# Optimization experiments

Hardware: AMD Instinct MI355X
Metric: run time of the kernel (lower is better)

Reference implementation:

```python
import jax, jax.numpy as jnp
import numpy as np

GROUP_SIZE = 32

def setup_inputs() -> dict:
    key = jax.random.key(0)
    k_x, k_w, k_b, k_se, k_zp = jax.random.split(key, 5)
    B, S, IN_CH, OUT_CH = 4, 2048, 4096, 4096
    n_groups = IN_CH // GROUP_SIZE
    x = jax.random.normal(k_x, (B, S, IN_CH), dtype=jnp.float32)
    weight = jax.random.normal(k_w, (OUT_CH, IN_CH), dtype=jnp.float32) * 0.02
    bias = jax.random.normal(k_b, (OUT_CH,), dtype=jnp.float32)
    # po2 scale: 2**e with int8 exponent; pick exponents so scale ~ weight magnitude / 15
    exp = jax.random.randint(k_se, (OUT_CH, n_groups, 1), -10, -6).astype(jnp.float32)
    weight_scale = jnp.exp2(exp)  # float32
    weight_zp = jax.random.randint(k_zp, (OUT_CH, n_groups, 1), 0, 16).astype(jnp.float32)
    return {"x": x, "weight": weight, "bias": bias,
            "weight_scale": weight_scale, "weight_zp": weight_zp}

def reference(x, weight, bias, weight_scale, weight_zp):
    out_ch, in_ch = weight.shape
    # [O, n_groups, group_size]
    w_g = weight.reshape(out_ch, in_ch // GROUP_SIZE, GROUP_SIZE)
    # asym uint4 quantize: clamp(round(w/scale + zp), 0, 15)
    q = jnp.clip(jnp.round(w_g / weight_scale + weight_zp), 0.0, 15.0)
    # dequantize: (q - zp) * scale, flatten groups back to [O, I]
    dq = ((q - weight_zp) * weight_scale).reshape(out_ch, in_ch)
    # F.linear: x @ dq.T + bias
    return jnp.einsum('bsi,oi->bso', x, dq) + bias
```

## Files before the change

### kernel.cpp

```cpp
#include <hip/hip_runtime.h>
#include <hip/hip_bf16.h>
#include <stdint.h>

typedef unsigned short ushort_t;
typedef __bf16 bf16x8 __attribute__((ext_vector_type(8)));
typedef float f32x4 __attribute__((ext_vector_type(4)));
typedef ushort_t ushort8v __attribute__((ext_vector_type(8)));


__device__ __forceinline__ ushort_t f2bf(float f) {
  unsigned int u = __float_as_uint(f);
  u += 0x7FFFu + ((u >> 16) & 1u);
  return (ushort_t)(u >> 16);
}

typedef __attribute__((address_space(1))) void gvoid_t;
typedef __attribute__((address_space(3))) void lvoid_t;

__device__ __forceinline__ void async_cp16(const ushort_t* g, ushort_t* l) {
  __builtin_amdgcn_global_load_lds((gvoid_t*)g, (lvoid_t*)l, 16, 0, 0);
}


__global__ __launch_bounds__(256) void cvt_x_kernel(const float4* __restrict__ x,
                                                    ushort8v* __restrict__ xb, int n8) {
  int i = blockIdx.x * 256 + threadIdx.x;
  if (i >= n8) return;
  float4 a = x[2 * i], b = x[2 * i + 1];
  ushort8v o;
  o[0] = f2bf(a.x); o[1] = f2bf(a.y); o[2] = f2bf(a.z); o[3] = f2bf(a.w);
  o[4] = f2bf(b.x); o[5] = f2bf(b.y); o[6] = f2bf(b.z); o[7] = f2bf(b.w);
  xb[i] = o;
}


__device__ __forceinline__ float dq1(float w, float rs, float s, float z) {
  float q = rintf(w * rs + z);
  q = fminf(fmaxf(q, 0.0f), 15.0f);
  return (q - z) * s;
}

__global__ __launch_bounds__(256) void dequant_w_kernel(const float* __restrict__ w,
                                                        const float* __restrict__ sc,
                                                        const float* __restrict__ zp,
                                                        ushort8v* __restrict__ wq, int n8) {
  int i = blockIdx.x * 256 + threadIdx.x;
  if (i >= n8) return;
  int base = i * 8;
  int gi = base >> 5;
  float s = sc[gi], z = zp[gi];
  float rs = 1.0f / s;
  const float4* w4 = (const float4*)(w + base);
  float4 a = w4[0], b = w4[1];
  ushort8v o;
  o[0] = f2bf(dq1(a.x, rs, s, z)); o[1] = f2bf(dq1(a.y, rs, s, z));
  o[2] = f2bf(dq1(a.z, rs, s, z)); o[3] = f2bf(dq1(a.w, rs, s, z));
  o[4] = f2bf(dq1(b.x, rs, s, z)); o[5] = f2bf(dq1(b.y, rs, s, z));
  o[6] = f2bf(dq1(b.z, rs, s, z)); o[7] = f2bf(dq1(b.w, rs, s, z));
  wq[i] = o;
}


#define BM 256
#define BN 256
#define BK 64

__device__ __forceinline__ f32x4 mfma16(bf16x8 a, bf16x8 b, f32x4 c) {
  return __builtin_amdgcn_mfma_f32_16x16x32_bf16(a, b, c, 0, 0, 0);
}

template <int MH, int NHB>
__device__ __forceinline__ void mfma_quad(f32x4 acc[2][4][4], const bf16x8 Afr[4][2],
                                          const bf16x8 Bfr[4][2]) {
#pragma unroll
  for (int k = 0; k < 2; ++k)
#pragma unroll
    for (int mt = 0; mt < 4; ++mt)
#pragma unroll
      for (int nt = 0; nt < 2; ++nt)
        acc[MH][mt][NHB * 2 + nt] =
            mfma16(Afr[mt][k], Bfr[NHB * 2 + nt][k], acc[MH][mt][NHB * 2 + nt]);
}

__global__ __launch_bounds__(512, 2) void gemm_bt_bias_kernel(
    const ushort_t* __restrict__ A,
    const ushort_t* __restrict__ B,
    const float* __restrict__ bias,
    float* __restrict__ C,
    int M, int N, int K) {
  __shared__ ushort_t sA[2][BM * BK];
  __shared__ ushort_t sB[2][BN * BK];

  const int tid  = threadIdx.x;
  const int wave = tid >> 6;
  const int lane = tid & 63;
  const int l15 = lane & 15, l4 = lane >> 4;

  int wg = blockIdx.x;
  const int nwg = gridDim.x;
  if ((nwg & 7) == 0) wg = (wg & 7) * (nwg >> 3) + (wg >> 3);
  const int nbn = N / BN;
  const int m0 = (wg / nbn) * BM, n0 = (wg % nbn) * BN;
  const int wm = (wave >> 2) * 128, wn = (wave & 3) * 64;

  const int srow = tid >> 3;
  const int scol = ((tid & 7) ^ (srow & 7)) * 8;
  const int ldst = wave * 64 * 8;

  const int xa  = l15 & 7;
  const int pc0 = (l4 ^ xa) << 3;
  const int pc1 = ((4 + l4) ^ xa) << 3;
  const int aoff = (wm + l15) * BK;
  const int boff = (wn + l15) * BK;

  f32x4 acc[2][4][4] = {};
  bf16x8 Afr[4][2], Bfr[4][2];

#define STAGE_A(sb, s, kn) \
  async_cp16(A + (size_t)(m0 + (s) * 64 + srow) * K + (kn) + scol, &sA[sb][(s) * 4096 + ldst])
#define STAGE_B(sb, s, kn) \
  async_cp16(B + (size_t)(n0 + (s) * 64 + srow) * K + (kn) + scol, &sB[sb][(s) * 4096 + ldst])
#define LDA(rb, mh, mt, k) \
  (*(const bf16x8*)&sA[rb][aoff + ((mh) * 64 + (mt) * 16) * BK + ((k) ? pc1 : pc0)])
#define LDB(rb, nt, k) \
  (*(const bf16x8*)&sB[rb][boff + (nt) * 16 * BK + ((k) ? pc1 : pc0)])
#define BAR()   __builtin_amdgcn_s_barrier()
#define LGKM0() asm volatile("s_waitcnt lgkmcnt(0)" ::: "memory")
#define VM(n)   asm volatile("s_waitcnt vmcnt(" #n ")" ::: "memory")
#define PRIO(p) __builtin_amdgcn_s_setprio(p)

  STAGE_B(0, 0, 0); STAGE_B(0, 1, 0); STAGE_A(0, 0, 0);
  STAGE_B(0, 2, 0); STAGE_B(0, 3, 0); STAGE_A(0, 2, 0);
  STAGE_A(0, 1, 0); STAGE_A(0, 3, 0);
  VM(2);
  BAR();

  const int nK = K / BK;
#pragma unroll 2
  for (int t = 0; t < nK - 1; ++t) {
    const int rb = t & 1, sb = rb ^ 1;
    const int kn = (t + 1) * BK;
#pragma unroll
    for (int mt = 0; mt < 4; ++mt) { Afr[mt][0] = LDA(rb, 0, mt, 0); Afr[mt][1] = LDA(rb, 0, mt, 1); }
#pragma unroll
    for (int nt = 0; nt < 2; ++nt) { Bfr[nt][0] = LDB(rb, nt, 0); Bfr[nt][1] = LDB(rb, nt, 1); }
    STAGE_B(sb, 0, kn); STAGE_B(sb, 1, kn); STAGE_A(sb, 0, kn);
    BAR(); LGKM0();
    PRIO(1); mfma_quad<0, 0>(acc, Afr, Bfr); PRIO(0);
    BAR();
#pragma unroll
    for (int nt = 2; nt < 4; ++nt) { Bfr[nt][0] = LDB(rb, nt, 0); Bfr[nt][1] = LDB(rb, nt, 1); }
    STAGE_B(sb, 2, kn); STAGE_B(sb, 3, kn); STAGE_A(sb, 2, kn);
    BAR(); LGKM0();
    PRIO(1); mfma_quad<0, 1>(acc, Afr, Bfr); PRIO(0);
    VM(6);
    BAR();
#pragma unroll
    for (int mt = 0; mt < 4; ++mt) { Afr[mt][0] = LDA(rb, 1, mt, 0); Afr[mt][1] = LDA(rb, 1, mt, 1); }
    STAGE_A(sb, 1, kn); STAGE_A(sb, 3, kn);
    BAR(); LGKM0();
    PRIO(1); mfma_quad<1, 0>(acc, Afr, Bfr); PRIO(0);
    BAR();
    PRIO(1); mfma_quad<1, 1>(acc, Afr, Bfr); PRIO(0);
    VM(2);
    BAR();
  }

  {
    const int rb = (nK - 1) & 1;
#pragma unroll
    for (int mt = 0; mt < 4; ++mt) { Afr[mt][0] = LDA(rb, 0, mt, 0); Afr[mt][1] = LDA(rb, 0, mt, 1); }
#pragma unroll
    for (int nt = 0; nt < 2; ++nt) { Bfr[nt][0] = LDB(rb, nt, 0); Bfr[nt][1] = LDB(rb, nt, 1); }
    BAR(); LGKM0();
    PRIO(1); mfma_quad<0, 0>(acc, Afr, Bfr); PRIO(0);
    BAR();
#pragma unroll
    for (int nt = 2; nt < 4; ++nt) { Bfr[nt][0] = LDB(rb, nt, 0); Bfr[nt][1] = LDB(rb, nt, 1); }
    BAR(); LGKM0();
    PRIO(1); mfma_quad<0, 1>(acc, Afr, Bfr); PRIO(0);
    VM(0);
    BAR();
#pragma unroll
    for (int mt = 0; mt < 4; ++mt) { Afr[mt][0] = LDA(rb, 1, mt, 0); Afr[mt][1] = LDA(rb, 1, mt, 1); }
    BAR(); LGKM0();
    PRIO(1); mfma_quad<1, 0>(acc, Afr, Bfr); PRIO(0);
    BAR();
    PRIO(1); mfma_quad<1, 1>(acc, Afr, Bfr); PRIO(0);
  }

  const int ccol = n0 + wn + l15;
  const int crow = m0 + wm + l4 * 4;
#pragma unroll
  for (int nt = 0; nt < 4; ++nt) {
    const float bv = bias[ccol + nt * 16];
#pragma unroll
    for (int mh = 0; mh < 2; ++mh)
#pragma unroll
      for (int mt = 0; mt < 4; ++mt)
#pragma unroll
        for (int r = 0; r < 4; ++r)
          C[(size_t)(crow + mh * 64 + mt * 16 + r) * N + ccol + nt * 16] =
              acc[mh][mt][nt][r] + bv;
  }
}


extern "C" void kernel_launch(void* const* d_in, const int* in_sizes, int n_in,
                              void* d_out, int out_size, void* d_ws, size_t ws_size,
                              hipStream_t stream) {
  const float* x    = (const float*)d_in[0];
  const float* w    = (const float*)d_in[1];
  const float* bias = (const float*)d_in[2];
  const float* sc   = (const float*)d_in[3];
  const float* zp   = (const float*)d_in[4];
  float* out = (float*)d_out;

  const int N = in_sizes[2];
  const int K = in_sizes[1] / N;
  const int M = in_sizes[0] / K;

  ushort_t* xb = (ushort_t*)d_ws;
  ushort_t* wq = xb + (size_t)M * K;

  int xn8 = (M * K) / 8;
  cvt_x_kernel<<<(xn8 + 255) / 256, 256, 0, stream>>>((const float4*)x, (ushort8v*)xb, xn8);

  int wn8 = (N * K) / 8;
  dequant_w_kernel<<<(wn8 + 255) / 256, 256, 0, stream>>>(w, sc, zp, (ushort8v*)wq, wn8);

  dim3 grid((M / BM) * (N / BN));
  gemm_bt_bias_kernel<<<grid, 512, 0, stream>>>(xb, wq, bias, out, M, N, K);
}
```

Baseline: 539.4 us.

## Prefetch two K-tiles ahead in GEMM and merge prep kernels into one

The GEMM main loop now issues global-to-LDS loads for tile t+2 into the buffer just consumed, instead of loading tile t+1 into the other buffer. This gives memory requests more time to land and reorders the vmcnt waits to match. The two preprocessing kernels are also merged into one grid-stride kernel with a fixed 2048-block grid, which removes a launch. A risk is that writing into the buffer currently being read depends on barrier placement; if that ordering is wrong it can race.

```diff
diff --git a/kernel.cpp b/kernel.cpp
--- a/kernel.cpp
+++ b/kernel.cpp
@@ -21,43 +21,42 @@
   __builtin_amdgcn_global_load_lds((gvoid_t*)g, (lvoid_t*)l, 16, 0, 0);
 }
 
-
-__global__ __launch_bounds__(256) void cvt_x_kernel(const float4* __restrict__ x,
-                                                    ushort8v* __restrict__ xb, int n8) {
-  int i = blockIdx.x * 256 + threadIdx.x;
-  if (i >= n8) return;
-  float4 a = x[2 * i], b = x[2 * i + 1];
-  ushort8v o;
-  o[0] = f2bf(a.x); o[1] = f2bf(a.y); o[2] = f2bf(a.z); o[3] = f2bf(a.w);
-  o[4] = f2bf(b.x); o[5] = f2bf(b.y); o[6] = f2bf(b.z); o[7] = f2bf(b.w);
-  xb[i] = o;
-}
-
-
 __device__ __forceinline__ float dq1(float w, float rs, float s, float z) {
   float q = rintf(w * rs + z);
   q = fminf(fmaxf(q, 0.0f), 15.0f);
   return (q - z) * s;
 }
 
-__global__ __launch_bounds__(256) void dequant_w_kernel(const float* __restrict__ w,
-                                                        const float* __restrict__ sc,
-                                                        const float* __restrict__ zp,
-                                                        ushort8v* __restrict__ wq, int n8) {
-  int i = blockIdx.x * 256 + threadIdx.x;
-  if (i >= n8) return;
-  int base = i * 8;
-  int gi = base >> 5;
-  float s = sc[gi], z = zp[gi];
-  float rs = 1.0f / s;
-  const float4* w4 = (const float4*)(w + base);
-  float4 a = w4[0], b = w4[1];
-  ushort8v o;
-  o[0] = f2bf(dq1(a.x, rs, s, z)); o[1] = f2bf(dq1(a.y, rs, s, z));
-  o[2] = f2bf(dq1(a.z, rs, s, z)); o[3] = f2bf(dq1(a.w, rs, s, z));
-  o[4] = f2bf(dq1(b.x, rs, s, z)); o[5] = f2bf(dq1(b.y, rs, s, z));
-  o[6] = f2bf(dq1(b.z, rs, s, z)); o[7] = f2bf(dq1(b.w, rs, s, z));
-  wq[i] = o;
+
+__global__ __launch_bounds__(256) void prep_kernel(
+    const float4* __restrict__ x, ushort8v* __restrict__ xb, int xn8,
+    const float* __restrict__ w, const float* __restrict__ sc,
+    const float* __restrict__ zp, ushort8v* __restrict__ wq, int wn8) {
+  const int total = xn8 + wn8;
+  const int stride = gridDim.x * 256;
+  for (int i = blockIdx.x * 256 + threadIdx.x; i < total; i += stride) {
+    if (i < xn8) {
+      float4 a = x[2 * i], b = x[2 * i + 1];
+      ushort8v o;
+      o[0] = f2bf(a.x); o[1] = f2bf(a.y); o[2] = f2bf(a.z); o[3] = f2bf(a.w);
+      o[4] = f2bf(b.x); o[5] = f2bf(b.y); o[6] = f2bf(b.z); o[7] = f2bf(b.w);
+      xb[i] = o;
+    } else {
+      int j = i - xn8;
+      int base = j * 8;
+      int gi = base >> 5;
+      float s = sc[gi], z = zp[gi];
+      float rs = 1.0f / s;
+      const float4* w4 = (const float4*)(w + base);
+      float4 a = w4[0], b = w4[1];
+      ushort8v o;
+      o[0] = f2bf(dq1(a.x, rs, s, z)); o[1] = f2bf(dq1(a.y, rs, s, z));
+      o[2] = f2bf(dq1(a.z, rs, s, z)); o[3] = f2bf(dq1(a.w, rs, s, z));
+      o[4] = f2bf(dq1(b.x, rs, s, z)); o[5] = f2bf(dq1(b.y, rs, s, z));
+      o[6] = f2bf(dq1(b.z, rs, s, z)); o[7] = f2bf(dq1(b.w, rs, s, z));
+      wq[j] = o;
+    }
+  }
 }
 
 
@@ -129,35 +128,64 @@
 #define VM(n)   asm volatile("s_waitcnt vmcnt(" #n ")" ::: "memory")
 #define PRIO(p) __builtin_amdgcn_s_setprio(p)
 
-  STAGE_B(0, 0, 0); STAGE_B(0, 1, 0); STAGE_A(0, 0, 0);
-  STAGE_B(0, 2, 0); STAGE_B(0, 3, 0); STAGE_A(0, 2, 0);
-  STAGE_A(0, 1, 0); STAGE_A(0, 3, 0);
-  VM(2);
+#define LOAD_A_MH0(rb) \
+  _Pragma("unroll") for (int mt = 0; mt < 4; ++mt) { Afr[mt][0] = LDA(rb, 0, mt, 0); Afr[mt][1] = LDA(rb, 0, mt, 1); }
+#define LOAD_A_MH1(rb) \
+  _Pragma("unroll") for (int mt = 0; mt < 4; ++mt) { Afr[mt][0] = LDA(rb, 1, mt, 0); Afr[mt][1] = LDA(rb, 1, mt, 1); }
+#define LOAD_B_LO(rb) \
+  _Pragma("unroll") for (int nt = 0; nt < 2; ++nt) { Bfr[nt][0] = LDB(rb, nt, 0); Bfr[nt][1] = LDB(rb, nt, 1); }
+#define LOAD_B_HI(rb) \
+  _Pragma("unroll") for (int nt = 2; nt < 4; ++nt) { Bfr[nt][0] = LDB(rb, nt, 0); Bfr[nt][1] = LDB(rb, nt, 1); }
+
+  STAGE_A(0, 0, 0);  STAGE_A(0, 2, 0);
+  STAGE_B(0, 0, 0);  STAGE_B(0, 1, 0);  STAGE_B(0, 2, 0);  STAGE_B(0, 3, 0);
+  STAGE_A(0, 1, 0);  STAGE_A(0, 3, 0);
+  STAGE_A(1, 0, BK); STAGE_A(1, 2, BK);
+  STAGE_B(1, 0, BK); STAGE_B(1, 1, BK); STAGE_B(1, 2, BK); STAGE_B(1, 3, BK);
+  STAGE_A(1, 1, BK); STAGE_A(1, 3, BK);
+  VM(10);
   BAR();
 
   const int nK = K / BK;
 #pragma unroll 2
-  for (int t = 0; t < nK - 1; ++t) {
-    const int rb = t & 1, sb = rb ^ 1;
-    const int kn = (t + 1) * BK;
-#pragma unroll
-    for (int mt = 0; mt < 4; ++mt) { Afr[mt][0] = LDA(rb, 0, mt, 0); Afr[mt][1] = LDA(rb, 0, mt, 1); }
-#pragma unroll
-    for (int nt = 0; nt < 2; ++nt) { Bfr[nt][0] = LDB(rb, nt, 0); Bfr[nt][1] = LDB(rb, nt, 1); }
-    STAGE_B(sb, 0, kn); STAGE_B(sb, 1, kn); STAGE_A(sb, 0, kn);
+  for (int t = 0; t < nK - 2; ++t) {
+    const int rb = t & 1;
+    const int kn2 = (t + 2) * BK;
+    LOAD_A_MH0(rb);
+    LOAD_B_LO(rb);
     BAR(); LGKM0();
     PRIO(1); mfma_quad<0, 0>(acc, Afr, Bfr); PRIO(0);
     BAR();
-#pragma unroll
-    for (int nt = 2; nt < 4; ++nt) { Bfr[nt][0] = LDB(rb, nt, 0); Bfr[nt][1] = LDB(rb, nt, 1); }
-    STAGE_B(sb, 2, kn); STAGE_B(sb, 3, kn); STAGE_A(sb, 2, kn);
+    LOAD_B_HI(rb);
+    STAGE_A(rb, 0, kn2); STAGE_A(rb, 2, kn2);
     BAR(); LGKM0();
     PRIO(1); mfma_quad<0, 1>(acc, Afr, Bfr); PRIO(0);
-    VM(6);
-    BAR();
-#pragma unroll
-    for (int mt = 0; mt < 4; ++mt) { Afr[mt][0] = LDA(rb, 1, mt, 0); Afr[mt][1] = LDA(rb, 1, mt, 1); }
-    STAGE_A(sb, 1, kn); STAGE_A(sb, 3, kn);
+    VM(10);
+    BAR();
+    LOAD_A_MH1(rb);
+    STAGE_B(rb, 0, kn2); STAGE_B(rb, 1, kn2); STAGE_B(rb, 2, kn2); STAGE_B(rb, 3, kn2);
+    BAR(); LGKM0();
+    PRIO(1); mfma_quad<1, 0>(acc, Afr, Bfr); PRIO(0);
+    BAR();
+    STAGE_A(rb, 1, kn2); STAGE_A(rb, 3, kn2);
+    PRIO(1); mfma_quad<1, 1>(acc, Afr, Bfr); PRIO(0);
+    VM(10);
+    BAR();
+  }
+
+  {
+    const int rb = (nK - 2) & 1;
+    LOAD_A_MH0(rb);
+    LOAD_B_LO(rb);
+    BAR(); LGKM0();
+    PRIO(1); mfma_quad<0, 0>(acc, Afr, Bfr); PRIO(0);
+    BAR();
+    LOAD_B_HI(rb);
+    BAR(); LGKM0();
+    PRIO(1); mfma_quad<0, 1>(acc, Afr, Bfr); PRIO(0);
+    VM(8);
+    BAR();
+    LOAD_A_MH1(rb);
     BAR(); LGKM0();
     PRIO(1); mfma_quad<1, 0>(acc, Afr, Bfr); PRIO(0);
     BAR();
@@ -165,24 +193,19 @@
     VM(2);
     BAR();
   }
-
   {
     const int rb = (nK - 1) & 1;
-#pragma unroll
-    for (int mt = 0; mt < 4; ++mt) { Afr[mt][0] = LDA(rb, 0, mt, 0); Afr[mt][1] = LDA(rb, 0, mt, 1); }
-#pragma unroll
-    for (int nt = 0; nt < 2; ++nt) { Bfr[nt][0] = LDB(rb, nt, 0); Bfr[nt][1] = LDB(rb, nt, 1); }
+    LOAD_A_MH0(rb);
+    LOAD_B_LO(rb);
     BAR(); LGKM0();
     PRIO(1); mfma_quad<0, 0>(acc, Afr, Bfr); PRIO(0);
     BAR();
-#pragma unroll
-    for (int nt = 2; nt < 4; ++nt) { Bfr[nt][0] = LDB(rb, nt, 0); Bfr[nt][1] = LDB(rb, nt, 1); }
+    LOAD_B_HI(rb);
     BAR(); LGKM0();
     PRIO(1); mfma_quad<0, 1>(acc, Afr, Bfr); PRIO(0);
     VM(0);
     BAR();
-#pragma unroll
-    for (int mt = 0; mt < 4; ++mt) { Afr[mt][0] = LDA(rb, 1, mt, 0); Afr[mt][1] = LDA(rb, 1, mt, 1); }
+    LOAD_A_MH1(rb);
     BAR(); LGKM0();
     PRIO(1); mfma_quad<1, 0>(acc, Afr, Bfr); PRIO(0);
     BAR();
@@ -224,10 +247,9 @@
   ushort_t* wq = xb + (size_t)M * K;
 
   int xn8 = (M * K) / 8;
-  cvt_x_kernel<<<(xn8 + 255) / 256, 256, 0, stream>>>((const float4*)x, (ushort8v*)xb, xn8);
-
   int wn8 = (N * K) / 8;
-  dequant_w_kernel<<<(wn8 + 255) / 256, 256, 0, stream>>>(w, sc, zp, (ushort8v*)wq, wn8);
+  prep_kernel<<<2048, 256, 0, stream>>>((const float4*)x, (ushort8v*)xb, xn8,
+                                        w, sc, zp, (ushort8v*)wq, wn8);
 
   dim3 grid((M / BM) * (N / BN));
   gemm_bt_bias_kernel<<<grid, 512, 0, stream>>>(xb, wq, bias, out, M, N, K);
```

Result: slower. 600.0 us (+11.2%).

## Simplify GEMM main loop to one barrier per K-step and widen conversion kernels

Applied to the files above, without the earlier changes.

The GEMM inner loop drops the fine-grained interleaving of partial async stages and multiple barriers per K tile. It now waits for all prior copies, does one barrier, issues the full next-tile prefetch, then loads fragments and runs all MFMA quads back to back. The x-convert and weight-dequant kernels each handle 16 elements per thread instead of 8, which halves the thread count. The simpler schedule removes barrier overhead but may expose global-load latency, since it waits on vmcnt(0) every iteration and no longer staggers LDS reads around the MFMAs.

```diff
diff --git a/kernel.cpp b/kernel.cpp
--- a/kernel.cpp
+++ b/kernel.cpp
@@ -23,14 +23,16 @@
 
 
 __global__ __launch_bounds__(256) void cvt_x_kernel(const float4* __restrict__ x,
-                                                    ushort8v* __restrict__ xb, int n8) {
+                                                    ushort8v* __restrict__ xb, int n16) {
   int i = blockIdx.x * 256 + threadIdx.x;
-  if (i >= n8) return;
-  float4 a = x[2 * i], b = x[2 * i + 1];
-  ushort8v o;
-  o[0] = f2bf(a.x); o[1] = f2bf(a.y); o[2] = f2bf(a.z); o[3] = f2bf(a.w);
-  o[4] = f2bf(b.x); o[5] = f2bf(b.y); o[6] = f2bf(b.z); o[7] = f2bf(b.w);
-  xb[i] = o;
+  if (i >= n16) return;
+  float4 a = x[4 * i], b = x[4 * i + 1], c = x[4 * i + 2], d = x[4 * i + 3];
+  ushort8v o0, o1;
+  o0[0] = f2bf(a.x); o0[1] = f2bf(a.y); o0[2] = f2bf(a.z); o0[3] = f2bf(a.w);
+  o0[4] = f2bf(b.x); o0[5] = f2bf(b.y); o0[6] = f2bf(b.z); o0[7] = f2bf(b.w);
+  o1[0] = f2bf(c.x); o1[1] = f2bf(c.y); o1[2] = f2bf(c.z); o1[3] = f2bf(c.w);
+  o1[4] = f2bf(d.x); o1[5] = f2bf(d.y); o1[6] = f2bf(d.z); o1[7] = f2bf(d.w);
+  xb[2 * i] = o0; xb[2 * i + 1] = o1;
 }
 
 
@@ -43,21 +45,26 @@
 __global__ __launch_bounds__(256) void dequant_w_kernel(const float* __restrict__ w,
                                                         const float* __restrict__ sc,
                                                         const float* __restrict__ zp,
-                                                        ushort8v* __restrict__ wq, int n8) {
+                                                        ushort8v* __restrict__ wq, int n16) {
   int i = blockIdx.x * 256 + threadIdx.x;
-  if (i >= n8) return;
-  int base = i * 8;
+  if (i >= n16) return;
+  int base = i * 16;
   int gi = base >> 5;
   float s = sc[gi], z = zp[gi];
   float rs = 1.0f / s;
   const float4* w4 = (const float4*)(w + base);
-  float4 a = w4[0], b = w4[1];
-  ushort8v o;
-  o[0] = f2bf(dq1(a.x, rs, s, z)); o[1] = f2bf(dq1(a.y, rs, s, z));
-  o[2] = f2bf(dq1(a.z, rs, s, z)); o[3] = f2bf(dq1(a.w, rs, s, z));
-  o[4] = f2bf(dq1(b.x, rs, s, z)); o[5] = f2bf(dq1(b.y, rs, s, z));
-  o[6] = f2bf(dq1(b.z, rs, s, z)); o[7] = f2bf(dq1(b.w, rs, s, z));
-  wq[i] = o;
+  float4 a = w4[0], b = w4[1], c = w4[2], d = w4[3];
+  ushort8v o0, o1;
+  o0[0] = f2bf(dq1(a.x, rs, s, z)); o0[1] = f2bf(dq1(a.y, rs, s, z));
+  o0[2] = f2bf(dq1(a.z, rs, s, z)); o0[3] = f2bf(dq1(a.w, rs, s, z));
+  o0[4] = f2bf(dq1(b.x, rs, s, z)); o0[5] = f2bf(dq1(b.y, rs, s, z));
+  o0[6] = f2bf(dq1(b.z, rs, s, z)); o0[7] = f2bf(dq1(b.w, rs, s, z));
+  o1[0] = f2bf(dq1(c.x, rs, s, z)); o1[1] = f2bf(dq1(c.y, rs, s, z));
+  o1[2] = f2bf(dq1(c.z, rs, s, z)); o1[3] = f2bf(dq1(c.w, rs, s, z));
+  o1[4] = f2bf(dq1(d.x, rs, s, z)); o1[5] = f2bf(dq1(d.y, rs, s, z));
+  o1[6] = f2bf(dq1(d.z, rs, s, z)); o1[7] = f2bf(dq1(d.w, rs, s, z));
+  ushort8v* out8 = (ushort8v*)wq + 2 * i;
+  out8[0] = o0; out8[1] = o1;
 }
 
 
@@ -120,72 +127,52 @@
   async_cp16(A + (size_t)(m0 + (s) * 64 + srow) * K + (kn) + scol, &sA[sb][(s) * 4096 + ldst])
 #define STAGE_B(sb, s, kn) \
   async_cp16(B + (size_t)(n0 + (s) * 64 + srow) * K + (kn) + scol, &sB[sb][(s) * 4096 + ldst])
+#define STAGE_ALL(sb, kn) do { \
+  STAGE_A(sb, 0, kn); STAGE_A(sb, 1, kn); STAGE_A(sb, 2, kn); STAGE_A(sb, 3, kn); \
+  STAGE_B(sb, 0, kn); STAGE_B(sb, 1, kn); STAGE_B(sb, 2, kn); STAGE_B(sb, 3, kn); \
+} while (0)
 #define LDA(rb, mh, mt, k) \
   (*(const bf16x8*)&sA[rb][aoff + ((mh) * 64 + (mt) * 16) * BK + ((k) ? pc1 : pc0)])
 #define LDB(rb, nt, k) \
   (*(const bf16x8*)&sB[rb][boff + (nt) * 16 * BK + ((k) ? pc1 : pc0)])
 #define BAR()   __builtin_amdgcn_s_barrier()
-#define LGKM0() asm volatile("s_waitcnt lgkmcnt(0)" ::: "memory")
-#define VM(n)   asm volatile("s_waitcnt vmcnt(" #n ")" ::: "memory")
+#define VM0()   asm volatile("s_waitcnt vmcnt(0)" ::: "memory")
 #define PRIO(p) __builtin_amdgcn_s_setprio(p)
 
-  STAGE_B(0, 0, 0); STAGE_B(0, 1, 0); STAGE_A(0, 0, 0);
-  STAGE_B(0, 2, 0); STAGE_B(0, 3, 0); STAGE_A(0, 2, 0);
-  STAGE_A(0, 1, 0); STAGE_A(0, 3, 0);
-  VM(2);
-  BAR();
+#define LOAD_A_MH0(rb) \
+  _Pragma("unroll") for (int mt = 0; mt < 4; ++mt) { Afr[mt][0] = LDA(rb, 0, mt, 0); Afr[mt][1] = LDA(rb, 0, mt, 1); }
+#define LOAD_A_MH1(rb) \
+  _Pragma("unroll") for (int mt = 0; mt < 4; ++mt) { Afr[mt][0] = LDA(rb, 1, mt, 0); Afr[mt][1] = LDA(rb, 1, mt, 1); }
+#define LOAD_B_ALL(rb) \
+  _Pragma("unroll") for (int nt = 0; nt < 4; ++nt) { Bfr[nt][0] = LDB(rb, nt, 0); Bfr[nt][1] = LDB(rb, nt, 1); }
+
+  STAGE_ALL(0, 0);
 
   const int nK = K / BK;
 #pragma unroll 2
   for (int t = 0; t < nK - 1; ++t) {
-    const int rb = t & 1, sb = rb ^ 1;
-    const int kn = (t + 1) * BK;
-#pragma unroll
-    for (int mt = 0; mt < 4; ++mt) { Afr[mt][0] = LDA(rb, 0, mt, 0); Afr[mt][1] = LDA(rb, 0, mt, 1); }
-#pragma unroll
-    for (int nt = 0; nt < 2; ++nt) { Bfr[nt][0] = LDB(rb, nt, 0); Bfr[nt][1] = LDB(rb, nt, 1); }
-    STAGE_B(sb, 0, kn); STAGE_B(sb, 1, kn); STAGE_A(sb, 0, kn);
-    BAR(); LGKM0();
+    const int rb = t & 1;
+    VM0();
+    BAR();
+    STAGE_ALL(rb ^ 1, (t + 1) * BK);
+    LOAD_A_MH0(rb);
+    LOAD_B_ALL(rb);
     PRIO(1); mfma_quad<0, 0>(acc, Afr, Bfr); PRIO(0);
-    BAR();
-#pragma unroll
-    for (int nt = 2; nt < 4; ++nt) { Bfr[nt][0] = LDB(rb, nt, 0); Bfr[nt][1] = LDB(rb, nt, 1); }
-    STAGE_B(sb, 2, kn); STAGE_B(sb, 3, kn); STAGE_A(sb, 2, kn);
-    BAR(); LGKM0();
     PRIO(1); mfma_quad<0, 1>(acc, Afr, Bfr); PRIO(0);
-    VM(6);
-    BAR();
-#pragma unroll
-    for (int mt = 0; mt < 4; ++mt) { Afr[mt][0] = LDA(rb, 1, mt, 0); Afr[mt][1] = LDA(rb, 1, mt, 1); }
-    STAGE_A(sb, 1, kn); STAGE_A(sb, 3, kn);
-    BAR(); LGKM0();
+    LOAD_A_MH1(rb);
     PRIO(1); mfma_quad<1, 0>(acc, Afr, Bfr); PRIO(0);
-    BAR();
     PRIO(1); mfma_quad<1, 1>(acc, Afr, Bfr); PRIO(0);
-    VM(2);
-    BAR();
   }
-
   {
     const int rb = (nK - 1) & 1;
-#pragma unroll
-    for (int mt = 0; mt < 4; ++mt) { Afr[mt][0] = LDA(rb, 0, mt, 0); Afr[mt][1] = LDA(rb, 0, mt, 1); }
-#pragma unroll
-    for (int nt = 0; nt < 2; ++nt) { Bfr[nt][0] = LDB(rb, nt, 0); Bfr[nt][1] = LDB(rb, nt, 1); }
-    BAR(); LGKM0();
+    VM0();
+    BAR();
+    LOAD_A_MH0(rb);
+    LOAD_B_ALL(rb);
     PRIO(1); mfma_quad<0, 0>(acc, Afr, Bfr); PRIO(0);
-    BAR();
-#pragma unroll
-    for (int nt = 2; nt < 4; ++nt) { Bfr[nt][0] = LDB(rb, nt, 0); Bfr[nt][1] = LDB(rb, nt, 1); }
-    BAR(); LGKM0();
     PRIO(1); mfma_quad<0, 1>(acc, Afr, Bfr); PRIO(0);
-    VM(0);
-    BAR();
-#pragma unroll
-    for (int mt = 0; mt < 4; ++mt) { Afr[mt][0] = LDA(rb, 1, mt, 0); Afr[mt][1] = LDA(rb, 1, mt, 1); }
-    BAR(); LGKM0();
+    LOAD_A_MH1(rb);
     PRIO(1); mfma_quad<1, 0>(acc, Afr, Bfr); PRIO(0);
-    BAR();
     PRIO(1); mfma_quad<1, 1>(acc, Afr, Bfr); PRIO(0);
   }
 
@@ -223,11 +210,11 @@
   ushort_t* xb = (ushort_t*)d_ws;
   ushort_t* wq = xb + (size_t)M * K;
 
-  int xn8 = (M * K) / 8;
-  cvt_x_kernel<<<(xn8 + 255) / 256, 256, 0, stream>>>((const float4*)x, (ushort8v*)xb, xn8);
-
-  int wn8 = (N * K) / 8;
-  dequant_w_kernel<<<(wn8 + 255) / 256, 256, 0, stream>>>(w, sc, zp, (ushort8v*)wq, wn8);
+  int xn16 = (M * K) / 16;
+  cvt_x_kernel<<<(xn16 + 255) / 256, 256, 0, stream>>>((const float4*)x, (ushort8v*)xb, xn16);
+
+  int wn16 = (N * K) / 16;
+  dequant_w_kernel<<<(wn16 + 255) / 256, 256, 0, stream>>>(w, sc, zp, (ushort8v*)wq, wn16);
 
   dim3 grid((M / BM) * (N / BN));
   gemm_bt_bias_kernel<<<grid, 512, 0, stream>>>(xb, wq, bias, out, M, N, K);
```

Result: slower. 568.6 us (+5.4%).

## Switch GEMM to 32x32x16 MFMA with 4 waves and 128x128 warp tiles

Applied to the files above, without the earlier changes.

Rewrites the bf16 GEMM main loop to use 32x32x16 MFMA instructions, with 256 threads per block and each wave owning a 128x128 output tile instead of 8 waves of 128x64. The K loop becomes a simpler double-buffered schedule: wait for all loads, barrier, issue the next tile's async copies, then interleave LDS fragment reads with MFMA groups using lgkmcnt waits and sched barriers. The aim is higher MFMA throughput per LDS byte read and fewer barriers per iteration. In exchange it needs many more accumulator registers (256 floats per lane) and runs only one block of 4 waves per CU, and the full vmcnt(0) wait at the top of each iteration reduces how much the global loads overlap with compute.

```diff
diff --git a/kernel.cpp b/kernel.cpp
--- a/kernel.cpp
+++ b/kernel.cpp
@@ -4,7 +4,7 @@
 
 typedef unsigned short ushort_t;
 typedef __bf16 bf16x8 __attribute__((ext_vector_type(8)));
-typedef float f32x4 __attribute__((ext_vector_type(4)));
+typedef float f32x16 __attribute__((ext_vector_type(16)));
 typedef ushort_t ushort8v __attribute__((ext_vector_type(8)));
 
 
@@ -65,24 +65,7 @@
 #define BN 256
 #define BK 64
 
-__device__ __forceinline__ f32x4 mfma16(bf16x8 a, bf16x8 b, f32x4 c) {
-  return __builtin_amdgcn_mfma_f32_16x16x32_bf16(a, b, c, 0, 0, 0);
-}
-
-template <int MH, int NHB>
-__device__ __forceinline__ void mfma_quad(f32x4 acc[2][4][4], const bf16x8 Afr[4][2],
-                                          const bf16x8 Bfr[4][2]) {
-#pragma unroll
-  for (int k = 0; k < 2; ++k)
-#pragma unroll
-    for (int mt = 0; mt < 4; ++mt)
-#pragma unroll
-      for (int nt = 0; nt < 2; ++nt)
-        acc[MH][mt][NHB * 2 + nt] =
-            mfma16(Afr[mt][k], Bfr[NHB * 2 + nt][k], acc[MH][mt][NHB * 2 + nt]);
-}
-
-__global__ __launch_bounds__(512, 2) void gemm_bt_bias_kernel(
+__global__ __launch_bounds__(256, 1) void gemm_bt_bias_kernel(
     const ushort_t* __restrict__ A,
     const ushort_t* __restrict__ B,
     const float* __restrict__ bias,
@@ -94,114 +77,104 @@
   const int tid  = threadIdx.x;
   const int wave = tid >> 6;
   const int lane = tid & 63;
-  const int l15 = lane & 15, l4 = lane >> 4;
+  const int l31 = lane & 31;
+  const int kb  = lane >> 5;
 
   int wg = blockIdx.x;
   const int nwg = gridDim.x;
   if ((nwg & 7) == 0) wg = (wg & 7) * (nwg >> 3) + (wg >> 3);
   const int nbn = N / BN;
   const int m0 = (wg / nbn) * BM, n0 = (wg % nbn) * BN;
-  const int wm = (wave >> 2) * 128, wn = (wave & 3) * 64;
+  const int wm = (wave >> 1) * 128, wn = (wave & 1) * 128;
 
   const int srow = tid >> 3;
   const int scol = ((tid & 7) ^ (srow & 7)) * 8;
-  const int ldst = wave * 64 * 8;
-
-  const int xa  = l15 & 7;
-  const int pc0 = (l4 ^ xa) << 3;
-  const int pc1 = ((4 + l4) ^ xa) << 3;
-  const int aoff = (wm + l15) * BK;
-  const int boff = (wn + l15) * BK;
-
-  f32x4 acc[2][4][4] = {};
-  bf16x8 Afr[4][2], Bfr[4][2];
+  const int ldst = wave * 512;
+
+  const int xa   = l31 & 7;
+  const int pcs0 = ((0 + kb) ^ xa) << 3;
+  const int pcs1 = ((2 + kb) ^ xa) << 3;
+  const int pcs2 = ((4 + kb) ^ xa) << 3;
+  const int pcs3 = ((6 + kb) ^ xa) << 3;
+  const int aoff = (wm + l31) * BK;
+  const int boff = (wn + l31) * BK;
+
+  f32x16 acc[4][4] = {};
+  bf16x8 FAe[4], FBe[4], FAo[4], FBo[4];
 
 #define STAGE_A(sb, s, kn) \
-  async_cp16(A + (size_t)(m0 + (s) * 64 + srow) * K + (kn) + scol, &sA[sb][(s) * 4096 + ldst])
+  async_cp16(A + (size_t)(m0 + (s) * 32 + srow) * K + (kn) + scol, &sA[sb][(s) * 2048 + ldst])
 #define STAGE_B(sb, s, kn) \
-  async_cp16(B + (size_t)(n0 + (s) * 64 + srow) * K + (kn) + scol, &sB[sb][(s) * 4096 + ldst])
-#define LDA(rb, mh, mt, k) \
-  (*(const bf16x8*)&sA[rb][aoff + ((mh) * 64 + (mt) * 16) * BK + ((k) ? pc1 : pc0)])
-#define LDB(rb, nt, k) \
-  (*(const bf16x8*)&sB[rb][boff + (nt) * 16 * BK + ((k) ? pc1 : pc0)])
-#define BAR()   __builtin_amdgcn_s_barrier()
-#define LGKM0() asm volatile("s_waitcnt lgkmcnt(0)" ::: "memory")
-#define VM(n)   asm volatile("s_waitcnt vmcnt(" #n ")" ::: "memory")
-#define PRIO(p) __builtin_amdgcn_s_setprio(p)
-
-  STAGE_B(0, 0, 0); STAGE_B(0, 1, 0); STAGE_A(0, 0, 0);
-  STAGE_B(0, 2, 0); STAGE_B(0, 3, 0); STAGE_A(0, 2, 0);
-  STAGE_A(0, 1, 0); STAGE_A(0, 3, 0);
-  VM(2);
-  BAR();
+  async_cp16(B + (size_t)(n0 + (s) * 32 + srow) * K + (kn) + scol, &sB[sb][(s) * 2048 + ldst])
+#define STAGE_ALL(sb, kn) do {                                              \
+  STAGE_A(sb, 0, kn); STAGE_A(sb, 1, kn); STAGE_A(sb, 2, kn); STAGE_A(sb, 3, kn); \
+  STAGE_A(sb, 4, kn); STAGE_A(sb, 5, kn); STAGE_A(sb, 6, kn); STAGE_A(sb, 7, kn); \
+  STAGE_B(sb, 0, kn); STAGE_B(sb, 1, kn); STAGE_B(sb, 2, kn); STAGE_B(sb, 3, kn); \
+  STAGE_B(sb, 4, kn); STAGE_B(sb, 5, kn); STAGE_B(sb, 6, kn); STAGE_B(sb, 7, kn); \
+} while (0)
+
+#define READ8(rb, PC, FA, FB) do {                                   \
+  const ushort_t* pa_ = &sA[rb][aoff + (PC)];                        \
+  const ushort_t* pb_ = &sB[rb][boff + (PC)];                        \
+  FA[0] = *(const bf16x8*)(pa_);                                     \
+  FA[1] = *(const bf16x8*)(pa_ + 2048);                              \
+  FA[2] = *(const bf16x8*)(pa_ + 4096);                              \
+  FA[3] = *(const bf16x8*)(pa_ + 6144);                              \
+  FB[0] = *(const bf16x8*)(pb_);                                     \
+  FB[1] = *(const bf16x8*)(pb_ + 2048);                              \
+  FB[2] = *(const bf16x8*)(pb_ + 4096);                              \
+  FB[3] = *(const bf16x8*)(pb_ + 6144);                              \
+} while (0)
+
+#define MFMA16(FA, FB)                                                       \
+  _Pragma("unroll") for (int mt = 0; mt < 4; ++mt)                           \
+  _Pragma("unroll") for (int nt = 0; nt < 4; ++nt)                           \
+      acc[mt][nt] = __builtin_amdgcn_mfma_f32_32x32x16_bf16(FA[mt], FB[nt],  \
+                                                            acc[mt][nt], 0, 0, 0);
+
+#define BAR()    __builtin_amdgcn_s_barrier()
+#define VM0()    asm volatile("s_waitcnt vmcnt(0)" ::: "memory")
+#define LGKM(n)  asm volatile("s_waitcnt lgkmcnt(" #n ")" ::: "memory")
+#define SB0()    __builtin_amdgcn_sched_barrier(0)
+
+  STAGE_ALL(0, 0);
 
   const int nK = K / BK;
 #pragma unroll 2
-  for (int t = 0; t < nK - 1; ++t) {
-    const int rb = t & 1, sb = rb ^ 1;
-    const int kn = (t + 1) * BK;
-#pragma unroll
-    for (int mt = 0; mt < 4; ++mt) { Afr[mt][0] = LDA(rb, 0, mt, 0); Afr[mt][1] = LDA(rb, 0, mt, 1); }
-#pragma unroll
-    for (int nt = 0; nt < 2; ++nt) { Bfr[nt][0] = LDB(rb, nt, 0); Bfr[nt][1] = LDB(rb, nt, 1); }
-    STAGE_B(sb, 0, kn); STAGE_B(sb, 1, kn); STAGE_A(sb, 0, kn);
-    BAR(); LGKM0();
-    PRIO(1); mfma_quad<0, 0>(acc, Afr, Bfr); PRIO(0);
+  for (int t = 0; t < nK; ++t) {
+    const int rb = t & 1;
+    VM0();
     BAR();
-#pragma unroll
-    for (int nt = 2; nt < 4; ++nt) { Bfr[nt][0] = LDB(rb, nt, 0); Bfr[nt][1] = LDB(rb, nt, 1); }
-    STAGE_B(sb, 2, kn); STAGE_B(sb, 3, kn); STAGE_A(sb, 2, kn);
-    BAR(); LGKM0();
-    PRIO(1); mfma_quad<0, 1>(acc, Afr, Bfr); PRIO(0);
-    VM(6);
-    BAR();
-#pragma unroll
-    for (int mt = 0; mt < 4; ++mt) { Afr[mt][0] = LDA(rb, 1, mt, 0); Afr[mt][1] = LDA(rb, 1, mt, 1); }
-    STAGE_A(sb, 1, kn); STAGE_A(sb, 3, kn);
-    BAR(); LGKM0();
-    PRIO(1); mfma_quad<1, 0>(acc, Afr, Bfr); PRIO(0);
-    BAR();
-    PRIO(1); mfma_quad<1, 1>(acc, Afr, Bfr); PRIO(0);
-    VM(2);
-    BAR();
+    READ8(rb, pcs0, FAe, FBe);
+    READ8(rb, pcs1, FAo, FBo);
+    if (t + 1 < nK) STAGE_ALL(rb ^ 1, (t + 1) * BK);
+    LGKM(8); SB0();
+    MFMA16(FAe, FBe);
+    READ8(rb, pcs2, FAe, FBe);
+    LGKM(8); SB0();
+    MFMA16(FAo, FBo);
+    READ8(rb, pcs3, FAo, FBo);
+    LGKM(8); SB0();
+    MFMA16(FAe, FBe);
+    LGKM(0); SB0();
+    MFMA16(FAo, FBo);
   }
 
-  {
-    const int rb = (nK - 1) & 1;
-#pragma unroll
-    for (int mt = 0; mt < 4; ++mt) { Afr[mt][0] = LDA(rb, 0, mt, 0); Afr[mt][1] = LDA(rb, 0, mt, 1); }
-#pragma unroll
-    for (int nt = 0; nt < 2; ++nt) { Bfr[nt][0] = LDB(rb, nt, 0); Bfr[nt][1] = LDB(rb, nt, 1); }
-    BAR(); LGKM0();
-    PRIO(1); mfma_quad<0, 0>(acc, Afr, Bfr); PRIO(0);
-    BAR();
-#pragma unroll
-    for (int nt = 2; nt < 4; ++nt) { Bfr[nt][0] = LDB(rb, nt, 0); Bfr[nt][1] = LDB(rb, nt, 1); }
-    BAR(); LGKM0();
-    PRIO(1); mfma_quad<0, 1>(acc, Afr, Bfr); PRIO(0);
-    VM(0);
-    BAR();
-#pragma unroll
-    for (int mt = 0; mt < 4; ++mt) { Afr[mt][0] = LDA(rb, 1, mt, 0); Afr[mt][1] = LDA(rb, 1, mt, 1); }
-    BAR(); LGKM0();
-    PRIO(1); mfma_quad<1, 0>(acc, Afr, Bfr); PRIO(0);
-    BAR();
-    PRIO(1); mfma_quad<1, 1>(acc, Afr, Bfr); PRIO(0);
-  }
-
-  const int ccol = n0 + wn + l15;
-  const int crow = m0 + wm + l4 * 4;
+  const int colbase = n0 + wn + l31;
 #pragma unroll
   for (int nt = 0; nt < 4; ++nt) {
-    const float bv = bias[ccol + nt * 16];
+    const int col = colbase + nt * 32;
+    const float bv = bias[col];
 #pragma unroll
-    for (int mh = 0; mh < 2; ++mh)
+    for (int mt = 0; mt < 4; ++mt) {
+      const int rowbase = m0 + wm + mt * 32 + 4 * kb;
+      const f32x16 v = acc[mt][nt];
 #pragma unroll
-      for (int mt = 0; mt < 4; ++mt)
-#pragma unroll
-        for (int r = 0; r < 4; ++r)
-          C[(size_t)(crow + mh * 64 + mt * 16 + r) * N + ccol + nt * 16] =
-              acc[mh][mt][nt][r] + bv;
+      for (int r = 0; r < 16; ++r) {
+        const int row = rowbase + (r & 3) + 8 * (r >> 2);
+        C[(size_t)row * N + col] = v[r] + bv;
+      }
+    }
   }
 }
 
@@ -230,5 +203,5 @@
   dequant_w_kernel<<<(wn8 + 255) / 256, 256, 0, stream>>>(w, sc, zp, (ushort8v*)wq, wn8);
 
   dim3 grid((M / BM) * (N / BN));
-  gemm_bt_bias_kernel<<<grid, 512, 0, stream>>>(xb, wq, bias, out, M, N, K);
-}
+  gemm_bt_bias_kernel<<<grid, 256, 0, stream>>>(xb, wq, bias, out, M, N, K);
+}
```

Result: slower. 555.9 us (+3.1%).
